# Optimization experiments

Measured on AMD Instinct MI355X. Metric: run time of the kernel, lower is better.

## Reference

```python
import jax, jax.numpy as jnp
import numpy as np

B, T, D, E, H, A, P, V, N = 64, 600, 512, 640, 1024, 1024, 1024, 10025, 64
ZH, ZC = 0.05, 0.05  # zoneout probs (eval: deterministic interpolation)


def setup_inputs() -> dict:
    key = jax.random.key(0)
    ks = jax.random.split(key, 18)
    def init(k, shape, fan_in):
        return jax.random.normal(k, shape, jnp.float32) / np.sqrt(fan_in)
    return {
        "encoder_outputs": jax.random.normal(ks[0], (B, T, D), jnp.float32),
        "labels": jax.random.randint(ks[1], (B, N), 0, V),
        "enc_seq_len": jax.random.randint(ks[2], (B,), 300, T + 1),
        "embed": init(ks[3], (V, E), 1.0) * 0.1,          # embedding table
        "W_ih": init(ks[4], (4 * H, E + D), E + D),        # LSTMCell input weights (i,f,g,o)
        "b_ih": init(ks[5], (4 * H,), H),
        "b_hh": init(ks[6], (4 * H,), H),
        "W_s": init(ks[7], (A, H), H),                     # s_transformed (no bias)
        "W_enc": init(ks[8], (A, D), D),                   # enc_ctx
        "b_enc": init(ks[9], (A,), D),
        "v_att": init(ks[10], (A,), A),                    # attention energy vector
        "W_fert": init(ks[11], (D,), D),                   # inv_fertility (no bias)
        "W_fb": init(ks[12], (A,), 1.0),                   # weight_feedback: Linear(1, A)
        "W_r": init(ks[13], (P, H + E + D), H + E + D),    # readout_in
        "b_r": init(ks[14], (P,), P),
        "W_o": init(ks[15], (V, P // 2), P // 2),          # output proj
        "b_o": init(ks[16], (V,), V),
    }


def reference(encoder_outputs, labels, enc_seq_len, embed, W_ih, b_ih, b_hh,
              W_s, W_enc, b_enc, v_att, W_fert, W_fb, W_r, b_r, W_o, b_o):
    # shifted target embeddings: pad zero in front, drop last  [B,N,E]
    emb = embed[labels]
    emb = jnp.pad(emb, ((0, 0), (1, 0), (0, 0)))[:, :-1, :]

    enc_ctx = encoder_outputs @ W_enc.T + b_enc                       # [B,T,A]
    inv_fert = jax.nn.sigmoid(encoder_outputs @ W_fert)               # [B,T]
    mask = jnp.arange(T)[None, :] < enc_seq_len[:, None]              # [B,T]
    bias = b_ih + b_hh

    def step(carry, emb_t):
        h, c, ctx, accum = carry                                      # accum: [B,T]
        x = jnp.concatenate([emb_t, ctx], axis=-1)                    # [B,E+D]
        # NOTE: source calls cell(inputs) with NO state -> LSTMCell uses zero h,c
        gates = x @ W_ih.T + bias                                     # [B,4H]
        i, f, g, o = jnp.split(gates, 4, axis=-1)
        c_new = jax.nn.sigmoid(i) * jnp.tanh(g)                       # f * 0 + i * g
        h_new = jax.nn.sigmoid(o) * jnp.tanh(c_new)
        h = ZH * h + (1.0 - ZH) * h_new                               # zoneout (eval)
        c = ZC * c + (1.0 - ZC) * c_new
        q = h @ W_s.T                                                 # [B,A]
        fb = accum[..., None] * W_fb[None, None, :]                   # [B,T,A]
        e = jnp.tanh(enc_ctx + q[:, None, :] + fb) @ v_att            # [B,T]
        e = jnp.where(mask, e, -jnp.inf)
        w = jax.nn.softmax(e, axis=1)                                 # [B,T]
        ctx = jnp.einsum('bt,btd->bd', w, encoder_outputs)            # [B,D]
        accum = accum + w * inv_fert * 0.5
        return (h, c, ctx, accum), (h, ctx)

    zeros_h = jnp.zeros((B, H), encoder_outputs.dtype)
    carry0 = (zeros_h, zeros_h,
              jnp.zeros((B, D), encoder_outputs.dtype),
              jnp.zeros((B, T), encoder_outputs.dtype))
    _, (s_seq, ctx_seq) = jax.lax.scan(step, carry0, jnp.swapaxes(emb, 0, 1))
    s = jnp.swapaxes(s_seq, 0, 1)                                     # [B,N,H]
    ctx_s = jnp.swapaxes(ctx_seq, 0, 1)                               # [B,N,D]

    r = jnp.concatenate([s, emb, ctx_s], axis=-1) @ W_r.T + b_r       # [B,N,P]
    r = r.reshape(B, N, P // 2, 2).max(axis=-1)                       # maxout(2)
    logits = r @ W_o.T + b_o                                          # [B,N,V]
    return logits
```

## Files before the change

### kernel.cpp

```cpp
#include <hip/hip_runtime.h>
#include <math.h>

constexpr int cB = 64, cT = 600, cD = 512, cE = 640, cH = 1024, cA = 1024,
              cP = 1024, cV = 10025, cN = 64;
constexpr int cBT = cB * cT;
constexpr int cKr = cH + cE + cD;
constexpr int cM  = cB * cN;
constexpr int cVp = 10112;
constexpr int cG3 = 3 * cH;
constexpr int cTQ = cT / 4;
constexpr int cXCS = 516;

typedef __attribute__((ext_vector_type(8))) short bf16x8;
typedef __attribute__((ext_vector_type(4))) float f32x4;

__device__ __forceinline__ float bfu(unsigned short s) {
  return __uint_as_float(((unsigned int)s) << 16);
}
__device__ __forceinline__ unsigned short f2bf(float f) {
  unsigned int x = __float_as_uint(f);
  x += 0x7fffu + ((x >> 16) & 1u);
  return (unsigned short)(x >> 16);
}
__device__ __forceinline__ float fsig(float x) { return 1.0f / (1.0f + __expf(-x)); }
__device__ __forceinline__ float ftanh(float x) {
  float e = __expf(2.0f * x);
  return 1.0f - 2.0f / (e + 1.0f);
}

#define GLD(g, s)                                                          \
  __builtin_amdgcn_global_load_lds(                                       \
      (const __attribute__((address_space(1))) void*)(g),                 \
      (__attribute__((address_space(3))) void*)(s), 16, 0, 0)

__device__ __forceinline__ int xcd_swizzle(int bid, int nwg) {
  int q = nwg >> 3, r = nwg & 7;
  int x = bid & 7, loc = bid >> 3;
  return (x < r ? x * (q + 1) : r * (q + 1) + (x - r) * q) + loc;
}

__device__ __forceinline__ void ast(float* p, float v) {
  __hip_atomic_store(p, v, __ATOMIC_RELAXED, __HIP_MEMORY_SCOPE_AGENT);
}
__device__ __forceinline__ float ald(const float* p) {
  return __hip_atomic_load(p, __ATOMIC_RELAXED, __HIP_MEMORY_SCOPE_AGENT);
}
__device__ __forceinline__ void arrive_wait(unsigned* c, unsigned target) {
  __syncthreads();
  if (threadIdx.x == 0) {
    __hip_atomic_fetch_add(c, 1u, __ATOMIC_RELEASE, __HIP_MEMORY_SCOPE_AGENT);
    while (__hip_atomic_load(c, __ATOMIC_ACQUIRE, __HIP_MEMORY_SCOPE_AGENT) < target)
      __builtin_amdgcn_s_sleep(2);
  }
  __syncthreads();
}


__global__ __launch_bounds__(256) void cast_kernel(const float* __restrict__ in,
                                                   unsigned short* __restrict__ out) {
  int i = blockIdx.x * 256 + threadIdx.x;
  float4 v = reinterpret_cast<const float4*>(in)[i];
  ushort4 o;
  o.x = f2bf(v.x); o.y = f2bf(v.y); o.z = f2bf(v.z); o.w = f2bf(v.w);
  reinterpret_cast<ushort4*>(out)[i] = o;
}

__global__ __launch_bounds__(256) void cast_hl_kernel(const float* __restrict__ in,
                                                      unsigned short* __restrict__ hi,
                                                      unsigned short* __restrict__ lo) {
  int i = blockIdx.x * 256 + threadIdx.x;
  float4 v = reinterpret_cast<const float4*>(in)[i];
  ushort4 h, l;
  h.x = f2bf(v.x); h.y = f2bf(v.y); h.z = f2bf(v.z); h.w = f2bf(v.w);
  l.x = f2bf(v.x - bfu(h.x)); l.y = f2bf(v.y - bfu(h.y));
  l.z = f2bf(v.z - bfu(h.z)); l.w = f2bf(v.w - bfu(h.w));
  reinterpret_cast<ushort4*>(hi)[i] = h;
  reinterpret_cast<ushort4*>(lo)[i] = l;
}

__global__ __launch_bounds__(256) void cast_wo_kernel(const float* __restrict__ in,
                                                      unsigned short* __restrict__ hi,
                                                      unsigned short* __restrict__ lo) {
  int idx = blockIdx.x * 256 + threadIdx.x;
  int row = idx >> 7;
  int k = (idx & 127) * 4;
  float4 v = (row < cV) ? *reinterpret_cast<const float4*>(&in[(size_t)row * cD + k])
                        : make_float4(0.f, 0.f, 0.f, 0.f);
  ushort4 h, l;
  h.x = f2bf(v.x); h.y = f2bf(v.y); h.z = f2bf(v.z); h.w = f2bf(v.w);
  l.x = f2bf(v.x - bfu(h.x)); l.y = f2bf(v.y - bfu(h.y));
  l.z = f2bf(v.z - bfu(h.z)); l.w = f2bf(v.w - bfu(h.w));
  reinterpret_cast<ushort4*>(hi)[idx] = h;
  reinterpret_cast<ushort4*>(lo)[idx] = l;
}

__global__ __launch_bounds__(256) void fert_kernel(const float* __restrict__ enc,
                                                   const float* __restrict__ W_fert,
                                                   float* __restrict__ inv_fert) {
  int wave = threadIdx.x >> 6, lane = threadIdx.x & 63;
  int row = blockIdx.x * 4 + wave;
  const float* r = enc + (size_t)row * cD;
  float s = 0.0f;
#pragma unroll
  for (int i = 0; i < 8; ++i) s += r[lane + 64 * i] * W_fert[lane + 64 * i];
#pragma unroll
  for (int o = 32; o; o >>= 1) s += __shfl_xor(s, o);
  if (lane == 0) inv_fert[row] = 1.0f / (1.0f + __expf(-s));
}

__global__ __launch_bounds__(256) void build_aemb(const float* __restrict__ embed,
                                                  const int* __restrict__ labels,
                                                  unsigned short* __restrict__ Ah,
                                                  unsigned short* __restrict__ Al) {
  int idx = blockIdx.x * 256 + threadIdx.x;
  int row = idx / (cE / 4);
  int k = (idx % (cE / 4)) * 4;
  int b = row >> 6, tt = row & 63;
  float4 v = make_float4(0.f, 0.f, 0.f, 0.f);
  if (tt > 0) {
    int lab = labels[b * cN + tt - 1];
    v = *reinterpret_cast<const float4*>(&embed[(size_t)lab * cE + k]);
  }
  ushort4 h, l;
  h.x = f2bf(v.x); h.y = f2bf(v.y); h.z = f2bf(v.z); h.w = f2bf(v.w);
  l.x = f2bf(v.x - bfu(h.x)); l.y = f2bf(v.y - bfu(h.y));
  l.z = f2bf(v.z - bfu(h.z)); l.w = f2bf(v.w - bfu(h.w));
  *reinterpret_cast<ushort4*>(&Ah[(size_t)row * cE + k]) = h;
  *reinterpret_cast<ushort4*>(&Al[(size_t)row * cE + k]) = l;
}

__global__ __launch_bounds__(256) void cast_wihe(const float* __restrict__ W_ih,
                                                 unsigned short* __restrict__ Wh,
                                                 unsigned short* __restrict__ Wl) {
  int idx = blockIdx.x * 256 + threadIdx.x;
  int jcol = idx / (cE / 4);
  int k = (idx % (cE / 4)) * 4;
  int r = (jcol < cH) ? jcol : jcol + cH;
  float4 v = *reinterpret_cast<const float4*>(&W_ih[(size_t)r * (cE + cD) + k]);
  ushort4 h, l;
  h.x = f2bf(v.x); h.y = f2bf(v.y); h.z = f2bf(v.z); h.w = f2bf(v.w);
  l.x = f2bf(v.x - bfu(h.x)); l.y = f2bf(v.y - bfu(h.y));
  l.z = f2bf(v.z - bfu(h.z)); l.w = f2bf(v.w - bfu(h.w));
  *reinterpret_cast<ushort4*>(&Wh[(size_t)jcol * cE + k]) = h;
  *reinterpret_cast<ushort4*>(&Wl[(size_t)jcol * cE + k]) = l;
}

__global__ __launch_bounds__(256) void pack_wih(const float* __restrict__ W_ih,
                                                unsigned short* __restrict__ WihP) {
  int idx = blockIdx.x * 256 + threadIdx.x;
  int col = idx >> 7;
  int k4 = idx & 127;
  int r = (col < cH) ? col : col + cH;
  float4 v = *reinterpret_cast<const float4*>(&W_ih[(size_t)r * (cE + cD) + cE + k4 * 4]);
  ushort4 h;
  h.x = f2bf(v.x); h.y = f2bf(v.y); h.z = f2bf(v.z); h.w = f2bf(v.w);
  *reinterpret_cast<ushort4*>(&WihP[((size_t)k4 * cG3 + col) * 4]) = h;
}

__global__ __launch_bounds__(256) void pack_ws(const float* __restrict__ W_s,
                                               unsigned short* __restrict__ WsP) {
  int idx = blockIdx.x * 256 + threadIdx.x;
  int a = idx >> 8;
  int k4 = idx & 255;
  float4 v = *reinterpret_cast<const float4*>(&W_s[(size_t)a * cH + k4 * 4]);
  ushort4 h;
  h.x = f2bf(v.x); h.y = f2bf(v.y); h.z = f2bf(v.z); h.w = f2bf(v.w);
  *reinterpret_cast<ushort4*>(&WsP[((size_t)k4 * cA + a) * 4]) = h;
}

__global__ __launch_bounds__(256) void build_ar_kernel(
    const float* __restrict__ s_seq, const float* __restrict__ ctx_seq,
    const float* __restrict__ embed, const int* __restrict__ labels,
    unsigned short* __restrict__ Ah, unsigned short* __restrict__ Al) {
  int idx = blockIdx.x * 256 + threadIdx.x;
  int row = idx / (cKr / 4);
  int k = (idx % (cKr / 4)) * 4;
  int b = row >> 6, tt = row & 63;
  float4 v;
  if (k < cH) {
    v = *reinterpret_cast<const float4*>(&s_seq[(size_t)row * cH + k]);
  } else if (k < cH + cE) {
    if (tt == 0) {
      v = make_float4(0.f, 0.f, 0.f, 0.f);
    } else {
      int lab = labels[b * cN + tt - 1];
      v = *reinterpret_cast<const float4*>(&embed[(size_t)lab * cE + (k - cH)]);
    }
  } else {
    v = *reinterpret_cast<const float4*>(&ctx_seq[(size_t)row * cD + (k - cH - cE)]);
  }
  ushort4 h, l;
  h.x = f2bf(v.x); h.y = f2bf(v.y); h.z = f2bf(v.z); h.w = f2bf(v.w);
  l.x = f2bf(v.x - bfu(h.x)); l.y = f2bf(v.y - bfu(h.y));
  l.z = f2bf(v.z - bfu(h.z)); l.w = f2bf(v.w - bfu(h.w));
  *reinterpret_cast<ushort4*>(&Ah[(size_t)row * cKr + k]) = h;
  *reinterpret_cast<ushort4*>(&Al[(size_t)row * cKr + k]) = l;
}


__global__ __launch_bounds__(256) void mfma_encctx(const unsigned short* __restrict__ A,
                                                   const unsigned short* __restrict__ Bm,
                                                   const float* __restrict__ bias,
                                                   unsigned short* __restrict__ C) {
  __shared__ unsigned short sA[4096], sB[4096];
  constexpr int nbx = cA / 128;
  int bid = xcd_swizzle(blockIdx.x, gridDim.x);
  int by = bid / nbx, bx = bid % nbx;
  int tid = threadIdx.x;
  int w = tid >> 6, l = tid & 63;
  int m0 = by * 128, n0 = bx * 128;
  int wr = w >> 1, wc = w & 1;
  f32x4 acc[4][4] = {};
  int srow = tid >> 2, scol = (tid & 3) * 8;
  for (int k0 = 0; k0 < cD; k0 += 32) {
    __syncthreads();
    GLD(&A[(size_t)(m0 + srow) * cD + k0 + scol], &sA[tid * 8]);
    GLD(&A[(size_t)(m0 + 64 + srow) * cD + k0 + scol], &sA[2048 + tid * 8]);
    GLD(&Bm[(size_t)(n0 + srow) * cD + k0 + scol], &sB[tid * 8]);
    GLD(&Bm[(size_t)(n0 + 64 + srow) * cD + k0 + scol], &sB[2048 + tid * 8]);
    __syncthreads();
    int rA = wr * 64 + (l & 15);
    int rB = wc * 64 + (l & 15);
    int kg = (l >> 4) * 8;
    bf16x8 a[4], b[4];
#pragma unroll
    for (int i = 0; i < 4; ++i) a[i] = *(const bf16x8*)&sA[(rA + i * 16) * 32 + kg];
#pragma unroll
    for (int j = 0; j < 4; ++j) b[j] = *(const bf16x8*)&sB[(rB + j * 16) * 32 + kg];
#pragma unroll
    for (int i = 0; i < 4; ++i)
#pragma unroll
      for (int j = 0; j < 4; ++j)
        acc[i][j] = __builtin_amdgcn_mfma_f32_16x16x32_bf16(a[i], b[j], acc[i][j], 0, 0, 0);
  }
  int rbase = m0 + wr * 64 + ((l >> 4) * 4);
  int cbase = n0 + wc * 64 + (l & 15);
  float bv[4];
#pragma unroll
  for (int j = 0; j < 4; ++j) bv[j] = bias[cbase + j * 16];
#pragma unroll
  for (int i = 0; i < 4; ++i)
#pragma unroll
    for (int q = 0; q < 4; ++q) {
      int row = rbase + i * 16 + q;
#pragma unroll
      for (int j = 0; j < 4; ++j) {
        int col = cbase + j * 16;
        int pos = (col < 512) ? (2 * col) : (2 * (col - 512) + 1);
        C[(size_t)row * cA + pos] = f2bf(acc[i][j][q] + bv[j]);
      }
    }
}

template <int EP>
__global__ __launch_bounds__(256) void mfma_gemm3(
    const unsigned short* __restrict__ Ah, const unsigned short* __restrict__ Al,
    const unsigned short* __restrict__ Bh, const unsigned short* __restrict__ Bl,
    const float* __restrict__ bias, void* __restrict__ outv, int K, int nbx) {
  __shared__ unsigned short sAh[4096], sAl[4096], sBh[4096], sBl[4096];
  int bid = xcd_swizzle(blockIdx.x, gridDim.x);
  int by = bid / nbx, bx = bid % nbx;
  int tid = threadIdx.x;
  int w = tid >> 6, l = tid & 63;
  int m0 = by * 128, n0 = bx * 128;
  int wr = w >> 1, wc = w & 1;
  f32x4 acc[4][4] = {};
  int srow = tid >> 2, scol = (tid & 3) * 8;
  for (int k0 = 0; k0 < K; k0 += 32) {
    __syncthreads();
    GLD(&Ah[(size_t)(m0 + srow) * K + k0 + scol], &sAh[tid * 8]);
    GLD(&Ah[(size_t)(m0 + 64 + srow) * K + k0 + scol], &sAh[2048 + tid * 8]);
    GLD(&Al[(size_t)(m0 + srow) * K + k0 + scol], &sAl[tid * 8]);
    GLD(&Al[(size_t)(m0 + 64 + srow) * K + k0 + scol], &sAl[2048 + tid * 8]);
    GLD(&Bh[(size_t)(n0 + srow) * K + k0 + scol], &sBh[tid * 8]);
    GLD(&Bh[(size_t)(n0 + 64 + srow) * K + k0 + scol], &sBh[2048 + tid * 8]);
    GLD(&Bl[(size_t)(n0 + srow) * K + k0 + scol], &sBl[tid * 8]);
    GLD(&Bl[(size_t)(n0 + 64 + srow) * K + k0 + scol], &sBl[2048 + tid * 8]);
    __syncthreads();
    int rA = wr * 64 + (l & 15);
    int rB = wc * 64 + (l & 15);
    int kg = (l >> 4) * 8;
    bf16x8 bh[4], bl[4];
#pragma unroll
    for (int j = 0; j < 4; ++j) {
      bh[j] = *(const bf16x8*)&sBh[(rB + j * 16) * 32 + kg];
      bl[j] = *(const bf16x8*)&sBl[(rB + j * 16) * 32 + kg];
    }
#pragma unroll
    for (int i = 0; i < 4; ++i) {
      bf16x8 ah = *(const bf16x8*)&sAh[(rA + i * 16) * 32 + kg];
      bf16x8 al = *(const bf16x8*)&sAl[(rA + i * 16) * 32 + kg];
#pragma unroll
      for (int j = 0; j < 4; ++j) {
        acc[i][j] = __builtin_amdgcn_mfma_f32_16x16x32_bf16(ah, bh[j], acc[i][j], 0, 0, 0);
        acc[i][j] = __builtin_amdgcn_mfma_f32_16x16x32_bf16(ah, bl[j], acc[i][j], 0, 0, 0);
        acc[i][j] = __builtin_amdgcn_mfma_f32_16x16x32_bf16(al, bh[j], acc[i][j], 0, 0, 0);
        if (EP == 2)
          acc[i][j] = __builtin_amdgcn_mfma_f32_16x16x32_bf16(al, bl[j], acc[i][j], 0, 0, 0);
      }
    }
  }
  int rbase = m0 + wr * 64 + ((l >> 4) * 4);
  int cbase = n0 + wc * 64 + (l & 15);
  if (EP == 0) {
    unsigned short* mo_h = (unsigned short*)outv;
    unsigned short* mo_l = mo_h + (size_t)cM * (cP / 2);
#pragma unroll
    for (int i = 0; i < 4; ++i)
#pragma unroll
      for (int q = 0; q < 4; ++q) {
        int row = rbase + i * 16 + q;
#pragma unroll
        for (int j = 0; j < 4; ++j) {
          float v = acc[i][j][q] + bias[cbase + j * 16];
          float o = fmaxf(v, __shfl_xor(v, 1));
          if (!(l & 1)) {
            int ch = (cbase + j * 16) >> 1;
            unsigned short h = f2bf(o);
            mo_h[(size_t)row * (cP / 2) + ch] = h;
            mo_l[(size_t)row * (cP / 2) + ch] = f2bf(o - bfu(h));
          }
        }
      }
  } else if (EP == 1) {
    float* out = (float*)outv;
#pragma unroll
    for (int i = 0; i < 4; ++i)
#pragma unroll
      for (int q = 0; q < 4; ++q) {
        int row = rbase + i * 16 + q;
#pragma unroll
        for (int j = 0; j < 4; ++j) {
          int col = cbase + j * 16;
          if (col < cV) out[(size_t)row * cV + col] = acc[i][j][q] + bias[col];
        }
      }
  } else {
    float* out = (float*)outv;
#pragma unroll
    for (int i = 0; i < 4; ++i)
#pragma unroll
      for (int q = 0; q < 4; ++q) {
        int row = rbase + i * 16 + q;
#pragma unroll
        for (int j = 0; j < 4; ++j)
          out[(size_t)row * cG3 + cbase + j * 16] = acc[i][j][q];
      }
  }
}


struct LoopArgs {
  const unsigned short* enc_ctx;
  const unsigned short* enc_bf;
  const unsigned short* WihP;
  const unsigned short* WsP;
  const float* b_ih;
  const float* b_hh;
  const float* embg;
  const float* inv_fert;
  const float* v_att;
  const float* W_fb;
  const int* slen;
  float* s_seq;
  float* ctx_seq;
  float* xq;
  float* xc;
  unsigned* cnt;
};

__global__ __launch_bounds__(1024)
__attribute__((amdgpu_waves_per_eu(4, 4)))
void split_loop(LoopArgs A) {
  __shared__ float ctx_s[cD];
  __shared__ float h_s[256];
  __shared__ float q_s[cA];
  __shared__ float ew_s[cTQ + 2];
  __shared__ float acc_s[cTQ];
  __shared__ float fert_s[cTQ];
  __shared__ float vatt_s[cA];
  __shared__ float wfb_s[cA];
  __shared__ float cpartL[4][256];
  __shared__ float cpartH[4][256];
  __shared__ float red_s[16];
  __shared__ float ms_s[8];

  const int xcd = blockIdx.x & 7, idx = blockIdx.x >> 3;
  const int qd = xcd >> 1;
  const int b = (xcd & 1) * 32 + idx;
  const int tid = threadIdx.x;
  const int wv = tid >> 6, ln = tid & 63;
  const int jl = tid >> 2, part = tid & 3;
  const int gp = tid >> 8;
  const int pp = tid & 255;
  const int q0 = qd * 256;
  const int len = A.slen[b];
  unsigned* cntQ = A.cnt + (0 * cB + b) * 64;
  unsigned* cntS = A.cnt + (1 * cB + b) * 64;

  if (tid < cD) ctx_s[tid] = 0.f;
  vatt_s[tid] = A.v_att[tid];
  wfb_s[tid] = A.W_fb[tid];
  if (tid < cTQ) {
    acc_s[tid] = 0.f;
    fert_s[tid] = A.inv_fert[b * cT + 4 * tid + qd];
  }
  if (tid >= cTQ && tid < cTQ + 2) ew_s[tid] = 0.f;
  float h_my = 0.f, bgi = 0.f, bgg = 0.f, bgo = 0.f;
  if (part == 0) {
    int j = q0 + jl;
    bgi = A.b_ih[j] + A.b_hh[j];
    bgg = A.b_ih[j + 2048] + A.b_hh[j + 2048];
    bgo = A.b_ih[j + 3072] + A.b_hh[j + 3072];
  }

  unsigned ec[4][8];
#pragma unroll
  for (int ip2 = 0; ip2 < 4; ++ip2) {
    int i = wv + 32 * ip2;
    const unsigned* rowp =
        (const unsigned*)(A.enc_ctx + (size_t)(b * cT + 4 * i + qd) * cA);
#pragma unroll
    for (int k2 = 0; k2 < 8; ++k2) ec[ip2][k2] = rowp[ln + 64 * k2];
  }

  unsigned ebr[38];
#pragma unroll
  for (int ii = 0; ii < 38; ++ii) {
    int i = gp + 4 * ii;
    ebr[ii] = (i < cTQ)
                  ? ((const unsigned*)(A.enc_bf + ((size_t)b * cT + 4 * i + qd) * cD))[pp]
                  : 0u;
  }
  __syncthreads();

  for (int t = 0; t < cN; ++t) {
    const int par = t & 1;
    const unsigned tgt = 4u * (t + 1);

    {
      float ai = 0.f, ag = 0.f, ao = 0.f;
      const unsigned short* wbase = A.WihP + (size_t)(q0 + jl) * 4;
#pragma unroll 4
      for (int k4 = 0; k4 < 32; ++k4) {
        int kk = (k4 + 2 * part) & 31;
        int row = part * 32 + kk;
        float4 c = *reinterpret_cast<const float4*>(&ctx_s[row * 4]);
        const unsigned short* pw = wbase + (size_t)row * (cG3 * 4);
        ushort4 wi = *reinterpret_cast<const ushort4*>(pw);
        ushort4 wg = *reinterpret_cast<const ushort4*>(pw + (size_t)1024 * 4);
        ushort4 wo = *reinterpret_cast<const ushort4*>(pw + (size_t)2048 * 4);
        ai += bfu(wi.x) * c.x + bfu(wi.y) * c.y + bfu(wi.z) * c.z + bfu(wi.w) * c.w;
        ag += bfu(wg.x) * c.x + bfu(wg.y) * c.y + bfu(wg.z) * c.z + bfu(wg.w) * c.w;
        ao += bfu(wo.x) * c.x + bfu(wo.y) * c.y + bfu(wo.z) * c.z + bfu(wo.w) * c.w;
      }
      ai += __shfl_xor(ai, 1); ai += __shfl_xor(ai, 2);
      ag += __shfl_xor(ag, 1); ag += __shfl_xor(ag, 2);
      ao += __shfl_xor(ao, 1); ao += __shfl_xor(ao, 2);
      if (part == 0) {
        int j = q0 + jl;
        const float* eg = A.embg + (size_t)(b * cN + t) * cG3;
        float gi = ai + bgi + eg[j];
        float gg = ag + bgg + eg[j + 1024];
        float go = ao + bgo + eg[j + 2048];
        float hnew = fsig(go) * ftanh(fsig(gi) * ftanh(gg));
        h_my = 0.05f * h_my + 0.95f * hnew;
        A.s_seq[(size_t)(b * cN + t) * cH + j] = h_my;
        h_s[jl] = h_my;
      }
    }
    __syncthreads();

    {
      float aq = 0.f;
      const unsigned short* pw = A.WsP + ((size_t)(qd * 64) * cA + tid) * 4;
#pragma unroll 8
      for (int kk = 0; kk < 64; ++kk) {
        float4 hh = *reinterpret_cast<const float4*>(&h_s[kk * 4]);
        ushort4 w = *reinterpret_cast<const ushort4*>(pw);
        aq += bfu(w.x) * hh.x + bfu(w.y) * hh.y + bfu(w.z) * hh.z + bfu(w.w) * hh.w;
        pw += (size_t)cA * 4;
      }
      ast(&A.xq[(((size_t)par * cB + b) * 4 + qd) * cA + tid], aq);
    }
    arrive_wait(cntQ, tgt);
    {
      const float* xb = A.xq + ((size_t)par * cB + b) * 4 * cA;
      q_s[tid] = ald(&xb[tid]) + ald(&xb[cA + tid]) + ald(&xb[2 * cA + tid]) +
                 ald(&xb[3 * cA + tid]);
    }
    __syncthreads();

#pragma unroll
    for (int ip = 0; ip < 10; ++ip) {
      int i = wv + 16 * ip;
      if (ip == 9 && i >= cTQ) continue;
      int tt = 4 * i + qd;
      if (tt >= len) {
        if (ln == 0) ew_s[i] = -__builtin_inff();
        continue;
      }
      float fb = acc_s[i];
      float acc = 0.f;
      if ((ip & 1) == 0 && ip < 8) {
        const int ip2 = ip >> 1;
#pragma unroll
        for (int k2 = 0; k2 < 8; ++k2) {
          unsigned u = ec[ip2][k2];
          int a0 = ln + 64 * k2;
          float c0 = __uint_as_float(u << 16);
          float c1 = __uint_as_float(u & 0xffff0000u);
          acc += vatt_s[a0] * ftanh(c0 + q_s[a0] + fb * wfb_s[a0]);
          acc += vatt_s[a0 + 512] * ftanh(c1 + q_s[a0 + 512] + fb * wfb_s[a0 + 512]);
        }
      } else {
        const unsigned* rowp =
            (const unsigned*)(A.enc_ctx + (size_t)(b * cT + tt) * cA);
#pragma unroll
        for (int k2 = 0; k2 < 8; ++k2) {
          unsigned u = rowp[ln + 64 * k2];
          int a0 = ln + 64 * k2;
          float c0 = __uint_as_float(u << 16);
          float c1 = __uint_as_float(u & 0xffff0000u);
          acc += vatt_s[a0] * ftanh(c0 + q_s[a0] + fb * wfb_s[a0]);
          acc += vatt_s[a0 + 512] * ftanh(c1 + q_s[a0 + 512] + fb * wfb_s[a0 + 512]);
        }
      }
#pragma unroll
      for (int o = 32; o; o >>= 1) acc += __shfl_xor(acc, o);
      if (ln == 0) ew_s[i] = acc;
    }
    __syncthreads();

    float m_loc;
    {
      float m = (tid < cTQ) ? ew_s[tid] : -__builtin_inff();
#pragma unroll
      for (int o = 32; o; o >>= 1) m = fmaxf(m, __shfl_xor(m, o));
      if (ln == 0) red_s[wv] = m;
      __syncthreads();
      m = red_s[0];
#pragma unroll
      for (int w2 = 1; w2 < 16; ++w2) m = fmaxf(m, red_s[w2]);
      m_loc = m;
      __syncthreads();
      float wn = 0.f;
      if (tid < cTQ) {
        float e = ew_s[tid];
        if (e > -__builtin_inff()) wn = __expf(e - m_loc);
        ew_s[tid] = wn;
      }
      float sp = wn;
#pragma unroll
      for (int o = 32; o; o >>= 1) sp += __shfl_xor(sp, o);
      if (ln == 0) red_s[wv] = sp;
      __syncthreads();
    }
    float s_loc = red_s[0];
#pragma unroll
    for (int w2 = 1; w2 < 16; ++w2) s_loc += red_s[w2];
    __syncthreads();

    {
      float s0 = 0.f, s1 = 0.f;
#pragma unroll
      for (int ii = 0; ii < 38; ++ii) {
        float wgt = ew_s[gp + 4 * ii];
        unsigned u = ebr[ii];
        s0 += wgt * __uint_as_float(u << 16);
        s1 += wgt * __uint_as_float(u & 0xffff0000u);
      }
      cpartL[gp][pp] = s0;
      cpartH[gp][pp] = s1;
    }
    __syncthreads();
    {
      float* xcb = A.xc + (((size_t)par * cB + b) * 4 + qd) * cXCS;
      if (tid < cD) {
        int p2 = tid >> 1;
        float v = (tid & 1)
                      ? (cpartH[0][p2] + cpartH[1][p2] + cpartH[2][p2] + cpartH[3][p2])
                      : (cpartL[0][p2] + cpartL[1][p2] + cpartL[2][p2] + cpartL[3][p2]);
        ast(&xcb[2 + tid], v);
      }
      if (tid == 0) ast(&xcb[0], m_loc);
      if (tid == 1) ast(&xcb[1], s_loc);
    }
    arrive_wait(cntS, tgt);

    if (tid < 8) {
      ms_s[tid] =
          ald(&A.xc[(((size_t)par * cB + b) * 4 + (tid >> 1)) * cXCS + (tid & 1)]);
    }
    __syncthreads();
    {
      float M = fmaxf(fmaxf(ms_s[0], ms_s[2]), fmaxf(ms_s[4], ms_s[6]));
      float sc0 = __expf(ms_s[0] - M), sc1 = __expf(ms_s[2] - M);
      float sc2 = __expf(ms_s[4] - M), sc3 = __expf(ms_s[6] - M);
      float tot = ms_s[1] * sc0 + ms_s[3] * sc1 + ms_s[5] * sc2 + ms_s[7] * sc3;
      float invt = 1.0f / tot;
      if (tid < cD) {
        const float* xcb = A.xc + ((size_t)par * cB + b) * 4 * cXCS;
        float cv = ald(&xcb[2 + tid]) * sc0 + ald(&xcb[cXCS + 2 + tid]) * sc1 +
                   ald(&xcb[2 * cXCS + 2 + tid]) * sc2 +
                   ald(&xcb[3 * cXCS + 2 + tid]) * sc3;
        cv *= invt;
        ctx_s[tid] = cv;
        if (qd == 0) A.ctx_seq[(size_t)(b * cN + t) * cD + tid] = cv;
      } else {
        int i = tid - 512;
        if (i < cTQ) {
          float scq = __expf(m_loc - M);
          acc_s[i] += ew_s[i] * scq * invt * fert_s[i] * 0.5f;
        }
      }
    }
    __syncthreads();
  }
}


extern "C" void kernel_launch(void* const* d_in, const int* in_sizes, int n_in,
                              void* d_out, int out_size, void* d_ws, size_t ws_size,
                              hipStream_t stream) {
  (void)in_sizes; (void)n_in; (void)out_size; (void)ws_size;
  const float* enc    = (const float*)d_in[0];
  const int*   labels = (const int*)d_in[1];
  const int*   slen   = (const int*)d_in[2];
  const float* embed  = (const float*)d_in[3];
  const float* W_ih   = (const float*)d_in[4];
  const float* b_ih   = (const float*)d_in[5];
  const float* b_hh   = (const float*)d_in[6];
  const float* W_s    = (const float*)d_in[7];
  const float* W_enc  = (const float*)d_in[8];
  const float* b_enc  = (const float*)d_in[9];
  const float* v_att  = (const float*)d_in[10];
  const float* W_fert = (const float*)d_in[11];
  const float* W_fb   = (const float*)d_in[12];
  const float* W_r    = (const float*)d_in[13];
  const float* b_r    = (const float*)d_in[14];
  const float* W_o    = (const float*)d_in[15];
  const float* b_o    = (const float*)d_in[16];
  float* out = (float*)d_out;

  char* ws = (char*)d_ws;
  size_t off = 0;
  auto alloc = [&](size_t bytes) -> char* {
    char* p = ws + off;
    off = (off + bytes + 255) & ~(size_t)255;
    return p;
  };
  unsigned short* enc_ctx = (unsigned short*)alloc((size_t)cBT * cA * 2);
  unsigned short* enc_bf  = (unsigned short*)alloc((size_t)cBT * cD * 2);
  unsigned short* wencb   = (unsigned short*)alloc((size_t)cA * cD * 2);
  float* inv_fert = (float*)alloc((size_t)cBT * 4);
  unsigned short* WihP = (unsigned short*)alloc((size_t)cD * cG3 * 2);
  unsigned short* WsP  = (unsigned short*)alloc((size_t)cH * cA * 2);
  float* embg     = (float*)alloc((size_t)cM * cG3 * 4);
  float* s_seq    = (float*)alloc((size_t)cM * cH * 4);
  float* ctx_seq  = (float*)alloc((size_t)cM * cD * 4);
  float* xq       = (float*)alloc((size_t)2 * cB * 4 * cA * 4);
  float* xc       = (float*)alloc((size_t)2 * cB * 4 * cXCS * 4);
  unsigned* cnt   = (unsigned*)alloc((size_t)2 * cB * 64 * 4);
  unsigned short* Aemb_h = (unsigned short*)alloc((size_t)cM * cE * 2);
  unsigned short* Aemb_l = (unsigned short*)alloc((size_t)cM * cE * 2);
  unsigned short* Wihe_h = (unsigned short*)alloc((size_t)cG3 * cE * 2);
  unsigned short* Wihe_l = (unsigned short*)alloc((size_t)cG3 * cE * 2);
  unsigned short* Ar_h = (unsigned short*)alloc((size_t)cM * cKr * 2);
  unsigned short* Ar_l = (unsigned short*)alloc((size_t)cM * cKr * 2);
  unsigned short* Wr_h = (unsigned short*)alloc((size_t)cP * cKr * 2);
  unsigned short* Wr_l = (unsigned short*)alloc((size_t)cP * cKr * 2);
  unsigned short* mo_hl = (unsigned short*)alloc((size_t)2 * cM * (cP / 2) * 2);
  unsigned short* Wo_h = (unsigned short*)alloc((size_t)cVp * cD * 2);
  unsigned short* Wo_l = (unsigned short*)alloc((size_t)cVp * cD * 2);

  hipMemsetAsync(cnt, 0, (size_t)2 * cB * 64 * 4, stream);

  cast_kernel<<<(cBT * cD) / 1024, 256, 0, stream>>>(enc, enc_bf);
  cast_kernel<<<(cA * cD) / 1024, 256, 0, stream>>>(W_enc, wencb);
  fert_kernel<<<cBT / 4, 256, 0, stream>>>(enc, W_fert, inv_fert);
  mfma_encctx<<<(cBT / 128) * (cA / 128), 256, 0, stream>>>(enc_bf, wencb, b_enc, enc_ctx);
  build_aemb<<<(cM * cE / 4) / 256, 256, 0, stream>>>(embed, labels, Aemb_h, Aemb_l);
  cast_wihe<<<(cG3 * cE / 4) / 256, 256, 0, stream>>>(W_ih, Wihe_h, Wihe_l);
  pack_wih<<<(cG3 * (cD / 4)) / 256, 256, 0, stream>>>(W_ih, WihP);
  pack_ws<<<(cA * (cH / 4)) / 256, 256, 0, stream>>>(W_s, WsP);
  cast_hl_kernel<<<(cP * cKr) / 1024, 256, 0, stream>>>(W_r, Wr_h, Wr_l);
  cast_wo_kernel<<<(cVp * cD) / 1024, 256, 0, stream>>>(W_o, Wo_h, Wo_l);
  mfma_gemm3<2><<<(cM / 128) * (cG3 / 128), 256, 0, stream>>>(
      Aemb_h, Aemb_l, Wihe_h, Wihe_l, nullptr, (void*)embg, cE, cG3 / 128);

  LoopArgs la;
  la.enc_ctx = enc_ctx; la.enc_bf = enc_bf; la.WihP = WihP; la.WsP = WsP;
  la.b_ih = b_ih; la.b_hh = b_hh; la.embg = embg; la.inv_fert = inv_fert;
  la.v_att = v_att; la.W_fb = W_fb; la.slen = slen;
  la.s_seq = s_seq; la.ctx_seq = ctx_seq;
  la.xq = xq; la.xc = xc; la.cnt = cnt;
  split_loop<<<dim3(256), dim3(1024), 0, stream>>>(la);

  build_ar_kernel<<<(cM * cKr) / 1024, 256, 0, stream>>>(s_seq, ctx_seq, embed, labels,
                                                         Ar_h, Ar_l);
  mfma_gemm3<0><<<(cM / 128) * (cP / 128), 256, 0, stream>>>(Ar_h, Ar_l, Wr_h, Wr_l, b_r,
                                                             (void*)mo_hl, cKr, cP / 128);
  unsigned short* mo_h = mo_hl;
  unsigned short* mo_l = mo_hl + (size_t)cM * (cP / 2);
  mfma_gemm3<1><<<(cM / 128) * (cVp / 128), 256, 0, stream>>>(mo_h, mo_l, Wo_h, Wo_l, b_o,
                                                              (void*)out, cP / 2, cVp / 128);
}
```

Measured before the change: 7.985 ms.

## Halve recurrent-loop block size to keep more encoder data in registers

The persistent attention/LSTM loop kernel now runs with 512 threads per block instead of 1024, using waves_per_eu 2. That gives each thread a larger register budget. Each thread caches 12 rows of enc_ctx and all 75 of its encoder-output rows in registers, so fewer rows must be re-read from global memory every step. Per-thread work in the gate, query, and context reductions doubles to cover the halved thread count. Fewer waves are available to hide latency, and the heavy register use risks spills.

Result: slower. 9.323 ms (median of 2 runs) (+16.8%).

```diff
diff --git a/kernel.cpp b/kernel.cpp
--- a/kernel.cpp
+++ b/kernel.cpp
@@ -10,6 +10,7 @@
 constexpr int cG3 = 3 * cH;
 constexpr int cTQ = cT / 4;
 constexpr int cXCS = 516;
+constexpr int cEC = 12;
 
 typedef __attribute__((ext_vector_type(8))) short bf16x8;
 typedef __attribute__((ext_vector_type(4))) float f32x4;
@@ -369,20 +370,20 @@
   unsigned* cnt;
 };
 
-__global__ __launch_bounds__(1024)
-__attribute__((amdgpu_waves_per_eu(4, 4)))
+__global__ __launch_bounds__(512)
+__attribute__((amdgpu_waves_per_eu(2, 2)))
 void split_loop(LoopArgs A) {
   __shared__ float ctx_s[cD];
   __shared__ float h_s[256];
   __shared__ float q_s[cA];
-  __shared__ float ew_s[cTQ + 2];
+  __shared__ float ew_s[cTQ];
   __shared__ float acc_s[cTQ];
   __shared__ float fert_s[cTQ];
   __shared__ float vatt_s[cA];
   __shared__ float wfb_s[cA];
-  __shared__ float cpartL[4][256];
-  __shared__ float cpartH[4][256];
-  __shared__ float red_s[16];
+  __shared__ float cpartL[2][256];
+  __shared__ float cpartH[2][256];
+  __shared__ float red_s[8];
   __shared__ float ms_s[8];
 
   const int xcd = blockIdx.x & 7, idx = blockIdx.x >> 3;
@@ -390,22 +391,22 @@
   const int b = (xcd & 1) * 32 + idx;
   const int tid = threadIdx.x;
   const int wv = tid >> 6, ln = tid & 63;
-  const int jl = tid >> 2, part = tid & 3;
-  const int gp = tid >> 8;
-  const int pp = tid & 255;
+  const int jl = tid >> 1, part = tid & 1;
+  const int gp2 = tid >> 8, pp = tid & 255;
   const int q0 = qd * 256;
   const int len = A.slen[b];
   unsigned* cntQ = A.cnt + (0 * cB + b) * 64;
   unsigned* cntS = A.cnt + (1 * cB + b) * 64;
 
-  if (tid < cD) ctx_s[tid] = 0.f;
-  vatt_s[tid] = A.v_att[tid];
-  wfb_s[tid] = A.W_fb[tid];
+  ctx_s[tid] = 0.f;
+  for (int i = tid; i < cA; i += 512) {
+    vatt_s[i] = A.v_att[i];
+    wfb_s[i] = A.W_fb[i];
+  }
   if (tid < cTQ) {
     acc_s[tid] = 0.f;
     fert_s[tid] = A.inv_fert[b * cT + 4 * tid + qd];
   }
-  if (tid >= cTQ && tid < cTQ + 2) ew_s[tid] = 0.f;
   float h_my = 0.f, bgi = 0.f, bgg = 0.f, bgo = 0.f;
   if (part == 0) {
     int j = q0 + jl;
@@ -414,24 +415,29 @@
     bgo = A.b_ih[j + 3072] + A.b_hh[j + 3072];
   }
 
-  unsigned ec[4][8];
-#pragma unroll
-  for (int ip2 = 0; ip2 < 4; ++ip2) {
-    int i = wv + 32 * ip2;
+  unsigned ec[cEC][8];
+#pragma unroll
+  for (int ip = 0; ip < cEC; ++ip) {
+    int i = wv + 8 * ip;
     const unsigned* rowp =
         (const unsigned*)(A.enc_ctx + (size_t)(b * cT + 4 * i + qd) * cA);
 #pragma unroll
-    for (int k2 = 0; k2 < 8; ++k2) ec[ip2][k2] = rowp[ln + 64 * k2];
-  }
-
-  unsigned ebr[38];
-#pragma unroll
-  for (int ii = 0; ii < 38; ++ii) {
-    int i = gp + 4 * ii;
-    ebr[ii] = (i < cTQ)
-                  ? ((const unsigned*)(A.enc_bf + ((size_t)b * cT + 4 * i + qd) * cD))[pp]
-                  : 0u;
-  }
+    for (int k2 = 0; k2 < 8; ++k2) ec[ip][k2] = rowp[ln + 64 * k2];
+  }
+#pragma unroll
+  for (int ip = 0; ip < cEC; ++ip)
+#pragma unroll
+    for (int k2 = 0; k2 < 8; ++k2) asm volatile("" : "+v"(ec[ip][k2]));
+
+  unsigned ebr[75];
+#pragma unroll
+  for (int ii = 0; ii < 75; ++ii) {
+    int i = gp2 + 2 * ii;
+    ebr[ii] =
+        ((const unsigned*)(A.enc_bf + ((size_t)b * cT + 4 * i + qd) * cD))[pp];
+  }
+#pragma unroll
+  for (int ii = 0; ii < 75; ++ii) asm volatile("" : "+v"(ebr[ii]));
   __syncthreads();
 
   for (int t = 0; t < cN; ++t) {
@@ -442,9 +448,9 @@
       float ai = 0.f, ag = 0.f, ao = 0.f;
       const unsigned short* wbase = A.WihP + (size_t)(q0 + jl) * 4;
 #pragma unroll 4
-      for (int k4 = 0; k4 < 32; ++k4) {
-        int kk = (k4 + 2 * part) & 31;
-        int row = part * 32 + kk;
+      for (int k4 = 0; k4 < 64; ++k4) {
+        int kk = (k4 + 4 * part) & 63;
+        int row = part * 64 + kk;
         float4 c = *reinterpret_cast<const float4*>(&ctx_s[row * 4]);
         const unsigned short* pw = wbase + (size_t)row * (cG3 * 4);
         ushort4 wi = *reinterpret_cast<const ushort4*>(pw);
@@ -454,9 +460,9 @@
         ag += bfu(wg.x) * c.x + bfu(wg.y) * c.y + bfu(wg.z) * c.z + bfu(wg.w) * c.w;
         ao += bfu(wo.x) * c.x + bfu(wo.y) * c.y + bfu(wo.z) * c.z + bfu(wo.w) * c.w;
       }
-      ai += __shfl_xor(ai, 1); ai += __shfl_xor(ai, 2);
-      ag += __shfl_xor(ag, 1); ag += __shfl_xor(ag, 2);
-      ao += __shfl_xor(ao, 1); ao += __shfl_xor(ao, 2);
+      ai += __shfl_xor(ai, 1);
+      ag += __shfl_xor(ag, 1);
+      ao += __shfl_xor(ao, 1);
       if (part == 0) {
         int j = q0 + jl;
         const float* eg = A.embg + (size_t)(b * cN + t) * cG3;
@@ -472,29 +478,37 @@
     __syncthreads();
 
     {
-      float aq = 0.f;
-      const unsigned short* pw = A.WsP + ((size_t)(qd * 64) * cA + tid) * 4;
+      float aq0 = 0.f, aq1 = 0.f;
+      const unsigned short* pw0 = A.WsP + ((size_t)(qd * 64) * cA + tid) * 4;
+      const unsigned short* pw1 = pw0 + (size_t)512 * 4;
 #pragma unroll 8
       for (int kk = 0; kk < 64; ++kk) {
         float4 hh = *reinterpret_cast<const float4*>(&h_s[kk * 4]);
-        ushort4 w = *reinterpret_cast<const ushort4*>(pw);
-        aq += bfu(w.x) * hh.x + bfu(w.y) * hh.y + bfu(w.z) * hh.z + bfu(w.w) * hh.w;
-        pw += (size_t)cA * 4;
-      }
-      ast(&A.xq[(((size_t)par * cB + b) * 4 + qd) * cA + tid], aq);
+        ushort4 w0 = *reinterpret_cast<const ushort4*>(pw0);
+        ushort4 w1 = *reinterpret_cast<const ushort4*>(pw1);
+        aq0 += bfu(w0.x) * hh.x + bfu(w0.y) * hh.y + bfu(w0.z) * hh.z + bfu(w0.w) * hh.w;
+        aq1 += bfu(w1.x) * hh.x + bfu(w1.y) * hh.y + bfu(w1.z) * hh.z + bfu(w1.w) * hh.w;
+        pw0 += (size_t)cA * 4;
+        pw1 += (size_t)cA * 4;
+      }
+      float* xb = A.xq + (((size_t)par * cB + b) * 4 + qd) * cA;
+      ast(&xb[tid], aq0);
+      ast(&xb[tid + 512], aq1);
     }
     arrive_wait(cntQ, tgt);
     {
       const float* xb = A.xq + ((size_t)par * cB + b) * 4 * cA;
       q_s[tid] = ald(&xb[tid]) + ald(&xb[cA + tid]) + ald(&xb[2 * cA + tid]) +
                  ald(&xb[3 * cA + tid]);
-    }
-    __syncthreads();
-
-#pragma unroll
-    for (int ip = 0; ip < 10; ++ip) {
-      int i = wv + 16 * ip;
-      if (ip == 9 && i >= cTQ) continue;
+      q_s[tid + 512] = ald(&xb[tid + 512]) + ald(&xb[cA + tid + 512]) +
+                       ald(&xb[2 * cA + tid + 512]) + ald(&xb[3 * cA + tid + 512]);
+    }
+    __syncthreads();
+
+#pragma unroll
+    for (int ip = 0; ip < 19; ++ip) {
+      int i = wv + 8 * ip;
+      if (ip == 18 && i >= cTQ) continue;
       int tt = 4 * i + qd;
       if (tt >= len) {
         if (ln == 0) ew_s[i] = -__builtin_inff();
@@ -502,11 +516,10 @@
       }
       float fb = acc_s[i];
       float acc = 0.f;
-      if ((ip & 1) == 0 && ip < 8) {
-        const int ip2 = ip >> 1;
+      if (ip < cEC) {
 #pragma unroll
         for (int k2 = 0; k2 < 8; ++k2) {
-          unsigned u = ec[ip2][k2];
+          unsigned u = ec[ip][k2];
           int a0 = ln + 64 * k2;
           float c0 = __uint_as_float(u << 16);
           float c1 = __uint_as_float(u & 0xffff0000u);
@@ -541,7 +554,7 @@
       __syncthreads();
       m = red_s[0];
 #pragma unroll
-      for (int w2 = 1; w2 < 16; ++w2) m = fmaxf(m, red_s[w2]);
+      for (int w2 = 1; w2 < 8; ++w2) m = fmaxf(m, red_s[w2]);
       m_loc = m;
       __syncthreads();
       float wn = 0.f;
@@ -558,31 +571,28 @@
     }
     float s_loc = red_s[0];
 #pragma unroll
-    for (int w2 = 1; w2 < 16; ++w2) s_loc += red_s[w2];
+    for (int w2 = 1; w2 < 8; ++w2) s_loc += red_s[w2];
     __syncthreads();
 
     {
       float s0 = 0.f, s1 = 0.f;
 #pragma unroll
-      for (int ii = 0; ii < 38; ++ii) {
-        float wgt = ew_s[gp + 4 * ii];
+      for (int ii = 0; ii < 75; ++ii) {
+        float wgt = ew_s[gp2 + 2 * ii];
         unsigned u = ebr[ii];
         s0 += wgt * __uint_as_float(u << 16);
         s1 += wgt * __uint_as_float(u & 0xffff0000u);
       }
-      cpartL[gp][pp] = s0;
-      cpartH[gp][pp] = s1;
+      cpartL[gp2][pp] = s0;
+      cpartH[gp2][pp] = s1;
     }
     __syncthreads();
     {
       float* xcb = A.xc + (((size_t)par * cB + b) * 4 + qd) * cXCS;
-      if (tid < cD) {
-        int p2 = tid >> 1;
-        float v = (tid & 1)
-                      ? (cpartH[0][p2] + cpartH[1][p2] + cpartH[2][p2] + cpartH[3][p2])
-                      : (cpartL[0][p2] + cpartL[1][p2] + cpartL[2][p2] + cpartL[3][p2]);
-        ast(&xcb[2 + tid], v);
-      }
+      int p2 = tid >> 1;
+      float v = (tid & 1) ? (cpartH[0][p2] + cpartH[1][p2])
+                          : (cpartL[0][p2] + cpartL[1][p2]);
+      ast(&xcb[2 + tid], v);
       if (tid == 0) ast(&xcb[0], m_loc);
       if (tid == 1) ast(&xcb[1], s_loc);
     }
@@ -599,7 +609,7 @@
       float sc2 = __expf(ms_s[4] - M), sc3 = __expf(ms_s[6] - M);
       float tot = ms_s[1] * sc0 + ms_s[3] * sc1 + ms_s[5] * sc2 + ms_s[7] * sc3;
       float invt = 1.0f / tot;
-      if (tid < cD) {
+      {
         const float* xcb = A.xc + ((size_t)par * cB + b) * 4 * cXCS;
         float cv = ald(&xcb[2 + tid]) * sc0 + ald(&xcb[cXCS + 2 + tid]) * sc1 +
                    ald(&xcb[2 * cXCS + 2 + tid]) * sc2 +
@@ -607,12 +617,10 @@
         cv *= invt;
         ctx_s[tid] = cv;
         if (qd == 0) A.ctx_seq[(size_t)(b * cN + t) * cD + tid] = cv;
-      } else {
-        int i = tid - 512;
-        if (i < cTQ) {
-          float scq = __expf(m_loc - M);
-          acc_s[i] += ew_s[i] * scq * invt * fert_s[i] * 0.5f;
-        }
+      }
+      if (tid < cTQ) {
+        float scq = __expf(m_loc - M);
+        acc_s[tid] += ew_s[tid] * scq * invt * fert_s[tid] * 0.5f;
       }
     }
     __syncthreads();
@@ -695,7 +703,7 @@
   la.v_att = v_att; la.W_fb = W_fb; la.slen = slen;
   la.s_seq = s_seq; la.ctx_seq = ctx_seq;
   la.xq = xq; la.xc = xc; la.cnt = cnt;
-  split_loop<<<dim3(256), dim3(1024), 0, stream>>>(la);
+  split_loop<<<dim3(256), dim3(512), 0, stream>>>(la);
 
   build_ar_kernel<<<(cM * cKr) / 1024, 256, 0, stream>>>(s_seq, ctx_seq, embed, labels,
                                                          Ar_h, Ar_l);
```

## Split each batch row's recurrent loop across eight blocks instead of four

Applied to the files above, without the earlier changes.

The persistent recurrent kernel now spreads each batch element over eight cooperating blocks (512 total) instead of four. Each block handles 128 hidden units, an eighth of the time steps and an eighth of the Ws contraction. Cross-block reductions for q and the softmax/context partials now combine eight partials. The register caches of enc_ctx and enc_bf rows are removed, so those are reread from global memory every step. This trades more sync participants and global reads for more parallelism per step and lower register pressure. Launch bounds change to allow 8 blocks per CU.

New measurement: 7.598 ms. -4.8%, faster.

```diff
diff --git a/kernel.cpp b/kernel.cpp
--- a/kernel.cpp
+++ b/kernel.cpp
@@ -8,8 +8,9 @@
 constexpr int cM  = cB * cN;
 constexpr int cVp = 10112;
 constexpr int cG3 = 3 * cH;
-constexpr int cTQ = cT / 4;
+constexpr int cTE = cT / 8;
 constexpr int cXCS = 516;
+constexpr int cNB = 8;
 
 typedef __attribute__((ext_vector_type(8))) short bf16x8;
 typedef __attribute__((ext_vector_type(4))) float f32x4;
@@ -369,31 +370,28 @@
   unsigned* cnt;
 };
 
-__global__ __launch_bounds__(1024)
-__attribute__((amdgpu_waves_per_eu(4, 4)))
+__global__ __launch_bounds__(1024, 8)
 void split_loop(LoopArgs A) {
   __shared__ float ctx_s[cD];
-  __shared__ float h_s[256];
+  __shared__ float h_s[128];
   __shared__ float q_s[cA];
-  __shared__ float ew_s[cTQ + 2];
-  __shared__ float acc_s[cTQ];
-  __shared__ float fert_s[cTQ];
+  __shared__ float ew_s[cTE + 5];
+  __shared__ float acc_s[cTE];
+  __shared__ float fert_s[cTE];
   __shared__ float vatt_s[cA];
   __shared__ float wfb_s[cA];
   __shared__ float cpartL[4][256];
   __shared__ float cpartH[4][256];
   __shared__ float red_s[16];
-  __shared__ float ms_s[8];
-
-  const int xcd = blockIdx.x & 7, idx = blockIdx.x >> 3;
-  const int qd = xcd >> 1;
-  const int b = (xcd & 1) * 32 + idx;
+  __shared__ float ms_s[16];
+
+  const int od = blockIdx.x & 7;
+  const int b = blockIdx.x >> 3;
   const int tid = threadIdx.x;
   const int wv = tid >> 6, ln = tid & 63;
-  const int jl = tid >> 2, part = tid & 3;
-  const int gp = tid >> 8;
-  const int pp = tid & 255;
-  const int q0 = qd * 256;
+  const int jl = tid >> 3, part = tid & 7;
+  const int gp = tid >> 8, pp = tid & 255;
+  const int j0 = od * 128;
   const int len = A.slen[b];
   unsigned* cntQ = A.cnt + (0 * cB + b) * 64;
   unsigned* cntS = A.cnt + (1 * cB + b) * 64;
@@ -401,50 +399,31 @@
   if (tid < cD) ctx_s[tid] = 0.f;
   vatt_s[tid] = A.v_att[tid];
   wfb_s[tid] = A.W_fb[tid];
-  if (tid < cTQ) {
+  if (tid < cTE) {
     acc_s[tid] = 0.f;
-    fert_s[tid] = A.inv_fert[b * cT + 4 * tid + qd];
-  }
-  if (tid >= cTQ && tid < cTQ + 2) ew_s[tid] = 0.f;
+    fert_s[tid] = A.inv_fert[b * cT + 8 * tid + od];
+  }
+  if (tid >= cTE && tid < cTE + 5) ew_s[tid] = 0.f;
   float h_my = 0.f, bgi = 0.f, bgg = 0.f, bgo = 0.f;
   if (part == 0) {
-    int j = q0 + jl;
+    int j = j0 + jl;
     bgi = A.b_ih[j] + A.b_hh[j];
     bgg = A.b_ih[j + 2048] + A.b_hh[j + 2048];
     bgo = A.b_ih[j + 3072] + A.b_hh[j + 3072];
   }
-
-  unsigned ec[4][8];
-#pragma unroll
-  for (int ip2 = 0; ip2 < 4; ++ip2) {
-    int i = wv + 32 * ip2;
-    const unsigned* rowp =
-        (const unsigned*)(A.enc_ctx + (size_t)(b * cT + 4 * i + qd) * cA);
-#pragma unroll
-    for (int k2 = 0; k2 < 8; ++k2) ec[ip2][k2] = rowp[ln + 64 * k2];
-  }
-
-  unsigned ebr[38];
-#pragma unroll
-  for (int ii = 0; ii < 38; ++ii) {
-    int i = gp + 4 * ii;
-    ebr[ii] = (i < cTQ)
-                  ? ((const unsigned*)(A.enc_bf + ((size_t)b * cT + 4 * i + qd) * cD))[pp]
-                  : 0u;
-  }
   __syncthreads();
 
   for (int t = 0; t < cN; ++t) {
     const int par = t & 1;
-    const unsigned tgt = 4u * (t + 1);
+    const unsigned tgt = (unsigned)cNB * (t + 1);
 
     {
       float ai = 0.f, ag = 0.f, ao = 0.f;
-      const unsigned short* wbase = A.WihP + (size_t)(q0 + jl) * 4;
+      const unsigned short* wbase = A.WihP + (size_t)(j0 + jl) * 4;
 #pragma unroll 4
-      for (int k4 = 0; k4 < 32; ++k4) {
-        int kk = (k4 + 2 * part) & 31;
-        int row = part * 32 + kk;
+      for (int k4 = 0; k4 < 16; ++k4) {
+        int kk = (k4 + 2 * part) & 15;
+        int row = part * 16 + kk;
         float4 c = *reinterpret_cast<const float4*>(&ctx_s[row * 4]);
         const unsigned short* pw = wbase + (size_t)row * (cG3 * 4);
         ushort4 wi = *reinterpret_cast<const ushort4*>(pw);
@@ -454,11 +433,11 @@
         ag += bfu(wg.x) * c.x + bfu(wg.y) * c.y + bfu(wg.z) * c.z + bfu(wg.w) * c.w;
         ao += bfu(wo.x) * c.x + bfu(wo.y) * c.y + bfu(wo.z) * c.z + bfu(wo.w) * c.w;
       }
-      ai += __shfl_xor(ai, 1); ai += __shfl_xor(ai, 2);
-      ag += __shfl_xor(ag, 1); ag += __shfl_xor(ag, 2);
-      ao += __shfl_xor(ao, 1); ao += __shfl_xor(ao, 2);
+      ai += __shfl_xor(ai, 1); ai += __shfl_xor(ai, 2); ai += __shfl_xor(ai, 4);
+      ag += __shfl_xor(ag, 1); ag += __shfl_xor(ag, 2); ag += __shfl_xor(ag, 4);
+      ao += __shfl_xor(ao, 1); ao += __shfl_xor(ao, 2); ao += __shfl_xor(ao, 4);
       if (part == 0) {
-        int j = q0 + jl;
+        int j = j0 + jl;
         const float* eg = A.embg + (size_t)(b * cN + t) * cG3;
         float gi = ai + bgi + eg[j];
         float gg = ag + bgg + eg[j + 1024];
@@ -473,58 +452,46 @@
 
     {
       float aq = 0.f;
-      const unsigned short* pw = A.WsP + ((size_t)(qd * 64) * cA + tid) * 4;
+      const unsigned short* pw = A.WsP + ((size_t)(od * 32) * cA + tid) * 4;
 #pragma unroll 8
-      for (int kk = 0; kk < 64; ++kk) {
+      for (int kk = 0; kk < 32; ++kk) {
         float4 hh = *reinterpret_cast<const float4*>(&h_s[kk * 4]);
         ushort4 w = *reinterpret_cast<const ushort4*>(pw);
         aq += bfu(w.x) * hh.x + bfu(w.y) * hh.y + bfu(w.z) * hh.z + bfu(w.w) * hh.w;
         pw += (size_t)cA * 4;
       }
-      ast(&A.xq[(((size_t)par * cB + b) * 4 + qd) * cA + tid], aq);
+      ast(&A.xq[(((size_t)par * cB + b) * cNB + od) * cA + tid], aq);
     }
     arrive_wait(cntQ, tgt);
     {
-      const float* xb = A.xq + ((size_t)par * cB + b) * 4 * cA;
-      q_s[tid] = ald(&xb[tid]) + ald(&xb[cA + tid]) + ald(&xb[2 * cA + tid]) +
-                 ald(&xb[3 * cA + tid]);
-    }
-    __syncthreads();
-
-#pragma unroll
-    for (int ip = 0; ip < 10; ++ip) {
+      const float* xb = A.xq + ((size_t)par * cB + b) * cNB * cA;
+      float s = 0.f;
+#pragma unroll
+      for (int o = 0; o < cNB; ++o) s += ald(&xb[o * cA + tid]);
+      q_s[tid] = s;
+    }
+    __syncthreads();
+
+#pragma unroll
+    for (int ip = 0; ip < 5; ++ip) {
       int i = wv + 16 * ip;
-      if (ip == 9 && i >= cTQ) continue;
-      int tt = 4 * i + qd;
+      if (ip == 4 && i >= cTE) continue;
+      int tt = 8 * i + od;
       if (tt >= len) {
         if (ln == 0) ew_s[i] = -__builtin_inff();
         continue;
       }
       float fb = acc_s[i];
+      const unsigned* rowp = (const unsigned*)(A.enc_ctx + (size_t)(b * cT + tt) * cA);
       float acc = 0.f;
-      if ((ip & 1) == 0 && ip < 8) {
-        const int ip2 = ip >> 1;
-#pragma unroll
-        for (int k2 = 0; k2 < 8; ++k2) {
-          unsigned u = ec[ip2][k2];
-          int a0 = ln + 64 * k2;
-          float c0 = __uint_as_float(u << 16);
-          float c1 = __uint_as_float(u & 0xffff0000u);
-          acc += vatt_s[a0] * ftanh(c0 + q_s[a0] + fb * wfb_s[a0]);
-          acc += vatt_s[a0 + 512] * ftanh(c1 + q_s[a0 + 512] + fb * wfb_s[a0 + 512]);
-        }
-      } else {
-        const unsigned* rowp =
-            (const unsigned*)(A.enc_ctx + (size_t)(b * cT + tt) * cA);
-#pragma unroll
-        for (int k2 = 0; k2 < 8; ++k2) {
-          unsigned u = rowp[ln + 64 * k2];
-          int a0 = ln + 64 * k2;
-          float c0 = __uint_as_float(u << 16);
-          float c1 = __uint_as_float(u & 0xffff0000u);
-          acc += vatt_s[a0] * ftanh(c0 + q_s[a0] + fb * wfb_s[a0]);
-          acc += vatt_s[a0 + 512] * ftanh(c1 + q_s[a0 + 512] + fb * wfb_s[a0 + 512]);
-        }
+#pragma unroll
+      for (int k2 = 0; k2 < 8; ++k2) {
+        unsigned u = rowp[ln + 64 * k2];
+        int a0 = ln + 64 * k2;
+        float c0 = __uint_as_float(u << 16);
+        float c1 = __uint_as_float(u & 0xffff0000u);
+        acc += vatt_s[a0] * ftanh(c0 + q_s[a0] + fb * wfb_s[a0]);
+        acc += vatt_s[a0 + 512] * ftanh(c1 + q_s[a0 + 512] + fb * wfb_s[a0 + 512]);
       }
 #pragma unroll
       for (int o = 32; o; o >>= 1) acc += __shfl_xor(acc, o);
@@ -534,7 +501,7 @@
 
     float m_loc;
     {
-      float m = (tid < cTQ) ? ew_s[tid] : -__builtin_inff();
+      float m = (tid < cTE) ? ew_s[tid] : -__builtin_inff();
 #pragma unroll
       for (int o = 32; o; o >>= 1) m = fmaxf(m, __shfl_xor(m, o));
       if (ln == 0) red_s[wv] = m;
@@ -545,7 +512,7 @@
       m_loc = m;
       __syncthreads();
       float wn = 0.f;
-      if (tid < cTQ) {
+      if (tid < cTE) {
         float e = ew_s[tid];
         if (e > -__builtin_inff()) wn = __expf(e - m_loc);
         ew_s[tid] = wn;
@@ -564,18 +531,22 @@
     {
       float s0 = 0.f, s1 = 0.f;
 #pragma unroll
-      for (int ii = 0; ii < 38; ++ii) {
-        float wgt = ew_s[gp + 4 * ii];
-        unsigned u = ebr[ii];
-        s0 += wgt * __uint_as_float(u << 16);
-        s1 += wgt * __uint_as_float(u & 0xffff0000u);
+      for (int ii = 0; ii < 19; ++ii) {
+        int i = gp + 4 * ii;
+        if (i < cTE) {
+          float wgt = ew_s[i];
+          unsigned u =
+              ((const unsigned*)(A.enc_bf + ((size_t)b * cT + 8 * i + od) * cD))[pp];
+          s0 += wgt * __uint_as_float(u << 16);
+          s1 += wgt * __uint_as_float(u & 0xffff0000u);
+        }
       }
       cpartL[gp][pp] = s0;
       cpartH[gp][pp] = s1;
     }
     __syncthreads();
     {
-      float* xcb = A.xc + (((size_t)par * cB + b) * 4 + qd) * cXCS;
+      float* xcb = A.xc + (((size_t)par * cB + b) * cNB + od) * cXCS;
       if (tid < cD) {
         int p2 = tid >> 1;
         float v = (tid & 1)
@@ -588,28 +559,34 @@
     }
     arrive_wait(cntS, tgt);
 
-    if (tid < 8) {
+    if (tid < 16) {
       ms_s[tid] =
-          ald(&A.xc[(((size_t)par * cB + b) * 4 + (tid >> 1)) * cXCS + (tid & 1)]);
+          ald(&A.xc[(((size_t)par * cB + b) * cNB + (tid >> 1)) * cXCS + (tid & 1)]);
     }
     __syncthreads();
     {
-      float M = fmaxf(fmaxf(ms_s[0], ms_s[2]), fmaxf(ms_s[4], ms_s[6]));
-      float sc0 = __expf(ms_s[0] - M), sc1 = __expf(ms_s[2] - M);
-      float sc2 = __expf(ms_s[4] - M), sc3 = __expf(ms_s[6] - M);
-      float tot = ms_s[1] * sc0 + ms_s[3] * sc1 + ms_s[5] * sc2 + ms_s[7] * sc3;
+      float M = -__builtin_inff();
+#pragma unroll
+      for (int o = 0; o < cNB; ++o) M = fmaxf(M, ms_s[2 * o]);
+      float tot = 0.f;
+      float sc[cNB];
+#pragma unroll
+      for (int o = 0; o < cNB; ++o) {
+        sc[o] = __expf(ms_s[2 * o] - M);
+        tot += ms_s[2 * o + 1] * sc[o];
+      }
       float invt = 1.0f / tot;
       if (tid < cD) {
-        const float* xcb = A.xc + ((size_t)par * cB + b) * 4 * cXCS;
-        float cv = ald(&xcb[2 + tid]) * sc0 + ald(&xcb[cXCS + 2 + tid]) * sc1 +
-                   ald(&xcb[2 * cXCS + 2 + tid]) * sc2 +
-                   ald(&xcb[3 * cXCS + 2 + tid]) * sc3;
+        const float* xcb = A.xc + ((size_t)par * cB + b) * cNB * cXCS;
+        float cv = 0.f;
+#pragma unroll
+        for (int o = 0; o < cNB; ++o) cv += ald(&xcb[o * cXCS + 2 + tid]) * sc[o];
         cv *= invt;
         ctx_s[tid] = cv;
-        if (qd == 0) A.ctx_seq[(size_t)(b * cN + t) * cD + tid] = cv;
+        if (od == 0) A.ctx_seq[(size_t)(b * cN + t) * cD + tid] = cv;
       } else {
         int i = tid - 512;
-        if (i < cTQ) {
+        if (i < cTE) {
           float scq = __expf(m_loc - M);
           acc_s[i] += ew_s[i] * scq * invt * fert_s[i] * 0.5f;
         }
@@ -659,8 +636,8 @@
   float* embg     = (float*)alloc((size_t)cM * cG3 * 4);
   float* s_seq    = (float*)alloc((size_t)cM * cH * 4);
   float* ctx_seq  = (float*)alloc((size_t)cM * cD * 4);
-  float* xq       = (float*)alloc((size_t)2 * cB * 4 * cA * 4);
-  float* xc       = (float*)alloc((size_t)2 * cB * 4 * cXCS * 4);
+  float* xq       = (float*)alloc((size_t)2 * cB * cNB * cA * 4);
+  float* xc       = (float*)alloc((size_t)2 * cB * cNB * cXCS * 4);
   unsigned* cnt   = (unsigned*)alloc((size_t)2 * cB * 64 * 4);
   unsigned short* Aemb_h = (unsigned short*)alloc((size_t)cM * cE * 2);
   unsigned short* Aemb_l = (unsigned short*)alloc((size_t)cM * cE * 2);
@@ -695,7 +672,7 @@
   la.v_att = v_att; la.W_fb = W_fb; la.slen = slen;
   la.s_seq = s_seq; la.ctx_seq = ctx_seq;
   la.xq = xq; la.xc = xc; la.cnt = cnt;
-  split_loop<<<dim3(256), dim3(1024), 0, stream>>>(la);
+  split_loop<<<dim3(cB * cNB), dim3(1024), 0, stream>>>(la);
 
   build_ar_kernel<<<(cM * cKr) / 1024, 256, 0, stream>>>(s_seq, ctx_seq, embed, labels,
                                                          Ar_h, Ar_l);
```
